# Optimization experiments

Hardware: AMD Instinct MI355X
Metric: run time of the kernel (lower is better)

Reference implementation:

```python
import jax, jax.numpy as jnp
import numpy as np

N_USERS = 6144
N_ITEMS = 12288
N_NODES = N_USERS + N_ITEMS
D = 64
AVG_DEG = 32
NNZ = N_NODES * AVG_DEG
N_LAYERS = 2
K = 30  # module keeps top (k+1) per row


def setup_inputs() -> dict:
    key = jax.random.key(0)
    k1, k2, k3, k4, k5 = jax.random.split(key, 5)
    user_emb = 0.1 * jax.random.normal(k1, (N_USERS, D), dtype=jnp.float32)
    item_emb = 0.1 * jax.random.normal(k2, (N_ITEMS, D), dtype=jnp.float32)
    edge_row = jax.random.randint(k3, (NNZ,), 0, N_NODES, dtype=jnp.int32)
    edge_col = jax.random.randint(k4, (NNZ,), 0, N_NODES, dtype=jnp.int32)
    # normalized-adjacency-like values (positive, ~1/deg scale)
    edge_val = jax.random.uniform(k5, (NNZ,), dtype=jnp.float32) / AVG_DEG
    return {
        "user_emb": user_emb,
        "item_emb": item_emb,
        "edge_row": edge_row,
        "edge_col": edge_col,
        "edge_val": edge_val,
    }


def _spmm(edge_row, edge_col, edge_val, x):
    # y[r] = sum_{(r,c) in E} val * x[c]   -- torch.sparse.mm equivalent (COO)
    return jax.ops.segment_sum(edge_val[:, None] * x[edge_col], edge_row,
                               num_segments=N_NODES)


def reference(user_emb, item_emb, edge_row, edge_col, edge_val):
    # LightGCN propagation
    all_emb = jnp.concatenate([user_emb, item_emb], axis=0)  # [N, D]
    embs = [all_emb]
    for _ in range(N_LAYERS):
        all_emb = _spmm(edge_row, edge_col, edge_val, all_emb)
        embs.append(all_emb)
    light_out = jnp.mean(jnp.stack(embs, axis=1), axis=1)  # [N, D]

    items = light_out[N_USERS:]  # [N_ITEMS, D]
    # F.normalize(dim=1, p=2) with eps clamp
    norm = jnp.linalg.norm(items, axis=1, keepdims=True)
    items = items / jnp.maximum(norm, 1e-12)

    # dense pairwise similarity
    sim = items @ items.T  # [N_ITEMS, N_ITEMS]

    # top_k: keep top (k+1) values per row, zero elsewhere
    vals, idx = jax.lax.top_k(sim, K + 1)  # [N_ITEMS, K+1]
    rows = jnp.arange(sim.shape[0])[:, None]
    sparse_sim = jnp.zeros_like(sim).at[rows, idx].set(vals)

    # apply_non_linearity('relu', i) -> relu
    return jax.nn.relu(sparse_sim)
```

## Files before the change

### kernel.cpp

```cpp
#include <hip/hip_runtime.h>
#include <hip/hip_bf16.h>

#define N_USERS 6144
#define N_ITEMS 12288
#define N_NODES 18432
#define D 64
#define NNZ 589824
#define K_TOP 31
#define NCAND_MIN 48
#define NCAND_MAX 240
#define CMAX 256

using frag_ab = __attribute__((ext_vector_type(8))) short;
using frag_cd = __attribute__((ext_vector_type(4))) float;

__device__ inline ushort f32_to_bf16_bits(float f) {
    unsigned b = __float_as_uint(f);
    unsigned r = (b + 0x7FFFu + ((b >> 16) & 1u)) >> 16;
    return (ushort)r;
}

__global__ void concat64_kernel(const float* __restrict__ u,
                                const float* __restrict__ it,
                                double* __restrict__ e0) {
    int i = blockIdx.x * 256 + threadIdx.x;
    const int NU = N_USERS * D;
    e0[i] = (i < NU) ? (double)u[i] : (double)it[i - NU];
}

__global__ void count_kernel(const int* __restrict__ er, int* __restrict__ cnt) {
    int e = blockIdx.x * 256 + threadIdx.x;
    atomicAdd(&cnt[er[e]], 1);
}

__global__ __launch_bounds__(256) void scan_kernel(const int* __restrict__ cnt,
                                                   int* __restrict__ row_start,
                                                   int* __restrict__ cursor) {
    __shared__ int part[256];
    int t = threadIdx.x;
    const int PER = N_NODES / 256;
    int s = 0;
    for (int i = 0; i < PER; ++i) s += cnt[t * PER + i];
    part[t] = s;
    __syncthreads();
    for (int off = 1; off < 256; off <<= 1) {
        int v = part[t];
        int w = (t >= off) ? part[t - off] : 0;
        __syncthreads();
        part[t] = v + w;
        __syncthreads();
    }
    int run = (t == 0) ? 0 : part[t - 1];
    for (int i = 0; i < PER; ++i) {
        int idx = t * PER + i;
        row_start[idx] = run;
        cursor[idx] = run;
        run += cnt[idx];
    }
    if (t == 255) row_start[N_NODES] = run;
}

__global__ void scatter_kernel(const int* __restrict__ er, const int* __restrict__ ec,
                               const float* __restrict__ ev,
                               int* __restrict__ cursor,
                               int* __restrict__ ecol_s, float* __restrict__ eval_s) {
    int e = blockIdx.x * 256 + threadIdx.x;
    int r = er[e];
    int pos = atomicAdd(&cursor[r], 1);
    ecol_s[pos] = ec[e];
    eval_s[pos] = ev[e];
}

__global__ __launch_bounds__(256) void spmm_csr_kernel(const int* __restrict__ row_start,
                                                       const int* __restrict__ ecol_s,
                                                       const float* __restrict__ eval_s,
                                                       const double* __restrict__ x,
                                                       double* __restrict__ y) {
    int t = threadIdx.x;
    int lane = t & 63, wave = t >> 6;
    int row = blockIdx.x * 4 + wave;
    if (row >= N_NODES) return;
    int beg = row_start[row], end = row_start[row + 1];
    double acc = 0.0;
    for (int j = beg; j < end; ++j) {
        int c = ecol_s[j];
        double v = (double)eval_s[j];
        acc += v * x[(size_t)c * D + lane];
    }
    y[(size_t)row * D + lane] = acc;
}

__global__ void mean_norm64_kernel(const double* __restrict__ e0,
                                   const double* __restrict__ e1,
                                   const double* __restrict__ e2,
                                   double* __restrict__ xn64,
                                   ushort* __restrict__ xh) {
    int t = threadIdx.x;
    int wave = t >> 6, lane = t & 63;
    int r = blockIdx.x * 4 + wave;
    size_t g = (size_t)(r + N_USERS) * D + lane;
    double s = (e0[g] + e1[g] + e2[g]) / 3.0;
    double ss = s * s;
    #pragma unroll
    for (int off = 32; off; off >>= 1) ss += __shfl_xor(ss, off);
    double norm = sqrt(ss);
    double denom = fmax(norm, 1e-12);
    double v = s / denom;
    xn64[(size_t)r * D + lane] = v;
    xh[(size_t)r * D + lane] = f32_to_bf16_bits((float)v);
}

#define LDS_STRIDE 72
__global__ __launch_bounds__(256) void simgemm_kernel(const ushort* __restrict__ Xh,
                                                      ushort* __restrict__ Cb) {
    __shared__ __align__(16) ushort Als[128 * LDS_STRIDE];
    __shared__ __align__(16) ushort Bls[128 * LDS_STRIDE];
    int t = threadIdx.x;
    int bi = blockIdx.y, bj = blockIdx.x;

    #pragma unroll
    for (int p = 0; p < 4; ++p) {
        int u4 = t + 256 * p;
        int row = u4 >> 3;
        int seg = u4 & 7;
        *(uint4*)&Als[row * LDS_STRIDE + seg * 8] =
            *(const uint4*)&Xh[(size_t)(bi * 128 + row) * D + seg * 8];
        *(uint4*)&Bls[row * LDS_STRIDE + seg * 8] =
            *(const uint4*)&Xh[(size_t)(bj * 128 + row) * D + seg * 8];
    }
    __syncthreads();

    int lane = t & 63, wave = t >> 6;
    int wrow = (wave >> 1) * 64, wcol = (wave & 1) * 64;
    int ml = lane & 15, quad = lane >> 4;

    frag_cd acc[4][4] = {};
    #pragma unroll
    for (int s = 0; s < 2; ++s) {
        frag_ab af[4], bf[4];
        int koff = s * 32 + quad * 8;
        #pragma unroll
        for (int rt = 0; rt < 4; ++rt)
            af[rt] = *(const frag_ab*)&Als[(wrow + rt * 16 + ml) * LDS_STRIDE + koff];
        #pragma unroll
        for (int ct = 0; ct < 4; ++ct)
            bf[ct] = *(const frag_ab*)&Bls[(wcol + ct * 16 + ml) * LDS_STRIDE + koff];
        #pragma unroll
        for (int rt = 0; rt < 4; ++rt)
            #pragma unroll
            for (int ct = 0; ct < 4; ++ct)
                acc[rt][ct] = __builtin_amdgcn_mfma_f32_16x16x32_bf16(
                    af[rt], bf[ct], acc[rt][ct], 0, 0, 0);
    }

    #pragma unroll
    for (int rt = 0; rt < 4; ++rt) {
        #pragma unroll
        for (int ct = 0; ct < 4; ++ct) {
            size_t gr = (size_t)(bi * 128 + wrow + rt * 16 + quad * 4);
            int    gc = bj * 128 + wcol + ct * 16 + ml;
            #pragma unroll
            for (int r = 0; r < 4; ++r)
                Cb[(gr + r) * N_ITEMS + gc] = f32_to_bf16_bits(acc[rt][ct][r]);
        }
    }
}

__global__ __launch_bounds__(256) void topk_kernel(const ushort* __restrict__ Cb,
                                                   float* __restrict__ Cout,
                                                   const double* __restrict__ xn64) {
    __shared__ int s_red[4];
    __shared__ unsigned s_cnt;
    __shared__ int    candi[CMAX];
    __shared__ double candv[CMAX];
    __shared__ double s_xr[D];
    int t = threadIdx.x;
    int r = blockIdx.x;
    const uint4* Crow4 = (const uint4*)(Cb + (size_t)r * N_ITEMS);

    unsigned short u[48];
    #pragma unroll
    for (int j = 0; j < 6; ++j) {
        uint4 f = Crow4[t + 256 * j];
        const unsigned* w = &f.x;
        #pragma unroll
        for (int q = 0; q < 4; ++q) {
            unsigned lo = w[q] & 0xFFFFu, hi = w[q] >> 16;
            u[j * 8 + 2 * q]     = (unsigned short)(lo ^ ((lo & 0x8000u) ? 0xFFFFu : 0x8000u));
            u[j * 8 + 2 * q + 1] = (unsigned short)(hi ^ ((hi & 0x8000u) ? 0xFFFFu : 0x8000u));
        }
    }
    if (t < D) s_xr[t] = xn64[(size_t)r * D + t];

    unsigned lo = 0u, hi = 0xFFFFu, T = 0u, bestT = 0u;
    int found = 0;
    for (int it = 0; it < 16; ++it) {
        if (found || lo > hi) { __syncthreads(); __syncthreads(); continue; }
        unsigned mid = lo + ((hi - lo) >> 1);
        int c = 0;
        #pragma unroll
        for (int k = 0; k < 48; ++k) c += (u[k] >= mid) ? 1 : 0;
        #pragma unroll
        for (int off = 32; off; off >>= 1) c += __shfl_down(c, off);
        if ((t & 63) == 0) s_red[t >> 6] = c;
        __syncthreads();
        int ctot = s_red[0] + s_red[1] + s_red[2] + s_red[3];
        __syncthreads();
        if (ctot >= NCAND_MIN) {
            bestT = mid;
            if (ctot <= NCAND_MAX) { T = mid; found = 1; }
            else lo = mid + 1;
        } else {
            if (mid == 0u) { lo = 1u; hi = 0u; }
            else hi = mid - 1;
        }
    }
    if (!found) T = bestT;

    if (t == 0) s_cnt = 0;
    __syncthreads();
    #pragma unroll
    for (int k = 0; k < 48; ++k) {
        if (u[k] >= (unsigned short)T) {
            unsigned pos = atomicAdd(&s_cnt, 1u);
            if (pos < CMAX) candi[pos] = 8 * (t + 256 * (k >> 3)) + (k & 7);
        }
    }
    __syncthreads();
    int c = (int)s_cnt; if (c > CMAX) c = CMAX;

    if (t < c) {
        const double* xc = xn64 + (size_t)candi[t] * D;
        double acc = 0.0;
        #pragma unroll 8
        for (int k = 0; k < D; ++k) acc += s_xr[k] * xc[k];
        candv[t] = acc;
    }
    __syncthreads();

    int   sel_idx = -1;
    float sel_val = 0.f;
    if (t < c) {
        double v = candv[t];
        int    id = candi[t];
        int rank = 0;
        for (int j = 0; j < c; ++j) {
            double vj = candv[j];
            rank += (vj > v || (vj == v && candi[j] < id)) ? 1 : 0;
        }
        if (rank < K_TOP) {
            sel_idx = id;
            sel_val = (v > 0.0) ? (float)v : 0.f;
        }
    }

    float4* Orow4 = (float4*)(Cout + (size_t)r * N_ITEMS);
    float4 z = make_float4(0.f, 0.f, 0.f, 0.f);
    #pragma unroll
    for (int j = 0; j < 12; ++j) Orow4[t + 256 * j] = z;
    __syncthreads();
    if (sel_idx >= 0) Cout[(size_t)r * N_ITEMS + sel_idx] = sel_val;
}

extern "C" void kernel_launch(void* const* d_in, const int* in_sizes, int n_in,
                              void* d_out, int out_size, void* d_ws, size_t ws_size,
                              hipStream_t stream) {
    const float* user_emb = (const float*)d_in[0];
    const float* item_emb = (const float*)d_in[1];
    const int*   edge_row = (const int*)d_in[2];
    const int*   edge_col = (const int*)d_in[3];
    const float* edge_val = (const float*)d_in[4];
    float* C = (float*)d_out;

    double* e0d  = (double*)d_ws;
    double* e1d  = e0d + (size_t)N_NODES * D;
    double* e2d  = e1d + (size_t)N_NODES * D;
    double* xn64 = e2d + (size_t)N_NODES * D;
    ushort* xh   = (ushort*)(xn64 + (size_t)N_ITEMS * D);
    ushort* Cb   = xh + (size_t)N_ITEMS * D;
    float*  eval_s = (float*)(Cb + (size_t)N_ITEMS * N_ITEMS);
    int*    ecol_s = (int*)(eval_s + NNZ);
    int*    cnt       = ecol_s + NNZ;
    int*    row_start = cnt + N_NODES;
    int*    cursor    = row_start + N_NODES + 1;

    hipMemsetAsync(cnt, 0, N_NODES * sizeof(int), stream);

    concat64_kernel<<<N_NODES * D / 256, 256, 0, stream>>>(user_emb, item_emb, e0d);

    count_kernel<<<NNZ / 256, 256, 0, stream>>>(edge_row, cnt);
    scan_kernel<<<1, 256, 0, stream>>>(cnt, row_start, cursor);
    scatter_kernel<<<NNZ / 256, 256, 0, stream>>>(edge_row, edge_col, edge_val,
                                                  cursor, ecol_s, eval_s);

    spmm_csr_kernel<<<(N_NODES + 3) / 4, 256, 0, stream>>>(row_start, ecol_s, eval_s, e0d, e1d);
    spmm_csr_kernel<<<(N_NODES + 3) / 4, 256, 0, stream>>>(row_start, ecol_s, eval_s, e1d, e2d);

    mean_norm64_kernel<<<N_ITEMS / 4, 256, 0, stream>>>(e0d, e1d, e2d, xn64, xh);

    dim3 ggrid(N_ITEMS / 128, N_ITEMS / 128);
    simgemm_kernel<<<ggrid, 256, 0, stream>>>(xh, Cb);

    topk_kernel<<<N_ITEMS, 256, 0, stream>>>(Cb, C, xn64);
}
```

Measured before the change: 1.004 ms.

## Pack edges, unroll SpMM, stage GEMM output via LDS, use nontemporal stores, early-exit search

Edge column and value are packed into one int2 array. The SpMM loop is unrolled by four with independent accumulators to raise memory-level parallelism. The similarity GEMM now writes its bf16 tile through LDS so that global stores are coalesced and nontemporal. The top-k kernel reads with nontemporal loads, zero-fills the output with nontemporal stores, and leaves the threshold binary search early, which is safe because the loop condition is uniform across the block. Splitting the sum into four accumulators changes the order of the double-precision additions slightly.

```diff
diff --git a/kernel.cpp b/kernel.cpp
--- a/kernel.cpp
+++ b/kernel.cpp
@@ -13,11 +13,13 @@
 
 using frag_ab = __attribute__((ext_vector_type(8))) short;
 using frag_cd = __attribute__((ext_vector_type(4))) float;
-
-__device__ inline ushort f32_to_bf16_bits(float f) {
+using uint4_e = __attribute__((ext_vector_type(4))) unsigned;
+using uint2_e = __attribute__((ext_vector_type(2))) unsigned;
+using float4_e = __attribute__((ext_vector_type(4))) float;
+
+__device__ inline unsigned f32_to_bf16_bits(float f) {
     unsigned b = __float_as_uint(f);
-    unsigned r = (b + 0x7FFFu + ((b >> 16) & 1u)) >> 16;
-    return (ushort)r;
+    return (b + 0x7FFFu + ((b >> 16) & 1u)) >> 16;
 }
 
 __global__ void concat64_kernel(const float* __restrict__ u,
@@ -62,18 +64,15 @@
 
 __global__ void scatter_kernel(const int* __restrict__ er, const int* __restrict__ ec,
                                const float* __restrict__ ev,
-                               int* __restrict__ cursor,
-                               int* __restrict__ ecol_s, float* __restrict__ eval_s) {
+                               int* __restrict__ cursor, int2* __restrict__ ep) {
     int e = blockIdx.x * 256 + threadIdx.x;
     int r = er[e];
     int pos = atomicAdd(&cursor[r], 1);
-    ecol_s[pos] = ec[e];
-    eval_s[pos] = ev[e];
+    ep[pos] = make_int2(ec[e], __float_as_int(ev[e]));
 }
 
 __global__ __launch_bounds__(256) void spmm_csr_kernel(const int* __restrict__ row_start,
-                                                       const int* __restrict__ ecol_s,
-                                                       const float* __restrict__ eval_s,
+                                                       const int2* __restrict__ ep,
                                                        const double* __restrict__ x,
                                                        double* __restrict__ y) {
     int t = threadIdx.x;
@@ -81,13 +80,21 @@
     int row = blockIdx.x * 4 + wave;
     if (row >= N_NODES) return;
     int beg = row_start[row], end = row_start[row + 1];
-    double acc = 0.0;
-    for (int j = beg; j < end; ++j) {
-        int c = ecol_s[j];
-        double v = (double)eval_s[j];
-        acc += v * x[(size_t)c * D + lane];
-    }
-    y[(size_t)row * D + lane] = acc;
+    double a0 = 0.0, a1 = 0.0, a2 = 0.0, a3 = 0.0;
+    int j = beg;
+    int n4 = beg + ((end - beg) & ~3);
+    for (; j < n4; j += 4) {
+        int2 p0 = ep[j], p1 = ep[j + 1], p2 = ep[j + 2], p3 = ep[j + 3];
+        a0 += (double)__int_as_float(p0.y) * x[(size_t)p0.x * D + lane];
+        a1 += (double)__int_as_float(p1.y) * x[(size_t)p1.x * D + lane];
+        a2 += (double)__int_as_float(p2.y) * x[(size_t)p2.x * D + lane];
+        a3 += (double)__int_as_float(p3.y) * x[(size_t)p3.x * D + lane];
+    }
+    for (; j < end; ++j) {
+        int2 p = ep[j];
+        a0 += (double)__int_as_float(p.y) * x[(size_t)p.x * D + lane];
+    }
+    y[(size_t)row * D + lane] = (a0 + a1) + (a2 + a3);
 }
 
 __global__ void mean_norm64_kernel(const double* __restrict__ e0,
@@ -107,14 +114,16 @@
     double denom = fmax(norm, 1e-12);
     double v = s / denom;
     xn64[(size_t)r * D + lane] = v;
-    xh[(size_t)r * D + lane] = f32_to_bf16_bits((float)v);
+    xh[(size_t)r * D + lane] = (ushort)f32_to_bf16_bits((float)v);
 }
 
 #define LDS_STRIDE 72
+#define OST_STRIDE 132
 __global__ __launch_bounds__(256) void simgemm_kernel(const ushort* __restrict__ Xh,
                                                       ushort* __restrict__ Cb) {
-    __shared__ __align__(16) ushort Als[128 * LDS_STRIDE];
-    __shared__ __align__(16) ushort Bls[128 * LDS_STRIDE];
+    __shared__ __align__(16) ushort S[2 * 128 * LDS_STRIDE];
+    ushort* Als = S;
+    ushort* Bls = S + 128 * LDS_STRIDE;
     int t = threadIdx.x;
     int bi = blockIdx.y, bj = blockIdx.x;
 
@@ -123,10 +132,10 @@
         int u4 = t + 256 * p;
         int row = u4 >> 3;
         int seg = u4 & 7;
-        *(uint4*)&Als[row * LDS_STRIDE + seg * 8] =
-            *(const uint4*)&Xh[(size_t)(bi * 128 + row) * D + seg * 8];
-        *(uint4*)&Bls[row * LDS_STRIDE + seg * 8] =
-            *(const uint4*)&Xh[(size_t)(bj * 128 + row) * D + seg * 8];
+        *(uint4_e*)&Als[row * LDS_STRIDE + seg * 8] =
+            *(const uint4_e*)&Xh[(size_t)(bi * 128 + row) * D + seg * 8];
+        *(uint4_e*)&Bls[row * LDS_STRIDE + seg * 8] =
+            *(const uint4_e*)&Xh[(size_t)(bj * 128 + row) * D + seg * 8];
     }
     __syncthreads();
 
@@ -152,17 +161,29 @@
                 acc[rt][ct] = __builtin_amdgcn_mfma_f32_16x16x32_bf16(
                     af[rt], bf[ct], acc[rt][ct], 0, 0, 0);
     }
-
+    __syncthreads();
+
+    ushort* Ost = S;
     #pragma unroll
     for (int rt = 0; rt < 4; ++rt) {
         #pragma unroll
         for (int ct = 0; ct < 4; ++ct) {
-            size_t gr = (size_t)(bi * 128 + wrow + rt * 16 + quad * 4);
-            int    gc = bj * 128 + wcol + ct * 16 + ml;
+            int row = wrow + rt * 16 + quad * 4;
+            int col = wcol + ct * 16 + ml;
             #pragma unroll
             for (int r = 0; r < 4; ++r)
-                Cb[(gr + r) * N_ITEMS + gc] = f32_to_bf16_bits(acc[rt][ct][r]);
-        }
+                Ost[(row + r) * OST_STRIDE + col] = (ushort)f32_to_bf16_bits(acc[rt][ct][r]);
+        }
+    }
+    __syncthreads();
+
+    const size_t base = (size_t)(bi * 128) * N_ITEMS + bj * 128;
+    #pragma unroll
+    for (int p = 0; p < 16; ++p) {
+        int i = t + 256 * p;
+        int row = i >> 5, cp = i & 31;
+        uint2_e v = *(const uint2_e*)&Ost[row * OST_STRIDE + cp * 4];
+        __builtin_nontemporal_store(v, (uint2_e*)(Cb + base + (size_t)row * N_ITEMS + cp * 4));
     }
 }
 
@@ -176,16 +197,16 @@
     __shared__ double s_xr[D];
     int t = threadIdx.x;
     int r = blockIdx.x;
-    const uint4* Crow4 = (const uint4*)(Cb + (size_t)r * N_ITEMS);
+    const uint4_e* Crow4 = (const uint4_e*)(Cb + (size_t)r * N_ITEMS);
 
     unsigned short u[48];
     #pragma unroll
     for (int j = 0; j < 6; ++j) {
-        uint4 f = Crow4[t + 256 * j];
-        const unsigned* w = &f.x;
+        uint4_e f = __builtin_nontemporal_load(&Crow4[t + 256 * j]);
         #pragma unroll
         for (int q = 0; q < 4; ++q) {
-            unsigned lo = w[q] & 0xFFFFu, hi = w[q] >> 16;
+            unsigned w = f[q];
+            unsigned lo = w & 0xFFFFu, hi = w >> 16;
             u[j * 8 + 2 * q]     = (unsigned short)(lo ^ ((lo & 0x8000u) ? 0xFFFFu : 0x8000u));
             u[j * 8 + 2 * q + 1] = (unsigned short)(hi ^ ((hi & 0x8000u) ? 0xFFFFu : 0x8000u));
         }
@@ -195,7 +216,6 @@
     unsigned lo = 0u, hi = 0xFFFFu, T = 0u, bestT = 0u;
     int found = 0;
     for (int it = 0; it < 16; ++it) {
-        if (found || lo > hi) { __syncthreads(); __syncthreads(); continue; }
         unsigned mid = lo + ((hi - lo) >> 1);
         int c = 0;
         #pragma unroll
@@ -211,9 +231,10 @@
             if (ctot <= NCAND_MAX) { T = mid; found = 1; }
             else lo = mid + 1;
         } else {
-            if (mid == 0u) { lo = 1u; hi = 0u; }
+            if (mid == 0u) { found = 1; T = bestT; }
             else hi = mid - 1;
         }
+        if (found || lo > hi) break;
     }
     if (!found) T = bestT;
 
@@ -254,10 +275,11 @@
         }
     }
 
-    float4* Orow4 = (float4*)(Cout + (size_t)r * N_ITEMS);
-    float4 z = make_float4(0.f, 0.f, 0.f, 0.f);
-    #pragma unroll
-    for (int j = 0; j < 12; ++j) Orow4[t + 256 * j] = z;
+    float4_e* Orow4 = (float4_e*)(Cout + (size_t)r * N_ITEMS);
+    float4_e z = {0.f, 0.f, 0.f, 0.f};
+    #pragma unroll
+    for (int j = 0; j < 12; ++j)
+        __builtin_nontemporal_store(z, &Orow4[t + 256 * j]);
     __syncthreads();
     if (sel_idx >= 0) Cout[(size_t)r * N_ITEMS + sel_idx] = sel_val;
 }
@@ -276,25 +298,23 @@
     double* e1d  = e0d + (size_t)N_NODES * D;
     double* e2d  = e1d + (size_t)N_NODES * D;
     double* xn64 = e2d + (size_t)N_NODES * D;
-    ushort* xh   = (ushort*)(xn64 + (size_t)N_ITEMS * D);
+    int2*   ep   = (int2*)(xn64 + (size_t)N_ITEMS * D);
+    ushort* xh   = (ushort*)(ep + NNZ);
     ushort* Cb   = xh + (size_t)N_ITEMS * D;
-    float*  eval_s = (float*)(Cb + (size_t)N_ITEMS * N_ITEMS);
-    int*    ecol_s = (int*)(eval_s + NNZ);
-    int*    cnt       = ecol_s + NNZ;
-    int*    row_start = cnt + N_NODES;
-    int*    cursor    = row_start + N_NODES + 1;
-
-    hipMemsetAsync(cnt, 0, N_NODES * sizeof(int), stream);
+    int*  cnt       = (int*)(Cb + (size_t)N_ITEMS * N_ITEMS);
+    int*  row_start = cnt + N_NODES;
+    int*  cursor    = row_start + N_NODES + 1;
+
+    (void)hipMemsetAsync(cnt, 0, N_NODES * sizeof(int), stream);
 
     concat64_kernel<<<N_NODES * D / 256, 256, 0, stream>>>(user_emb, item_emb, e0d);
 
     count_kernel<<<NNZ / 256, 256, 0, stream>>>(edge_row, cnt);
     scan_kernel<<<1, 256, 0, stream>>>(cnt, row_start, cursor);
-    scatter_kernel<<<NNZ / 256, 256, 0, stream>>>(edge_row, edge_col, edge_val,
-                                                  cursor, ecol_s, eval_s);
-
-    spmm_csr_kernel<<<(N_NODES + 3) / 4, 256, 0, stream>>>(row_start, ecol_s, eval_s, e0d, e1d);
-    spmm_csr_kernel<<<(N_NODES + 3) / 4, 256, 0, stream>>>(row_start, ecol_s, eval_s, e1d, e2d);
+    scatter_kernel<<<NNZ / 256, 256, 0, stream>>>(edge_row, edge_col, edge_val, cursor, ep);
+
+    spmm_csr_kernel<<<(N_NODES + 3) / 4, 256, 0, stream>>>(row_start, ep, e0d, e1d);
+    spmm_csr_kernel<<<(N_NODES + 3) / 4, 256, 0, stream>>>(row_start, ep, e1d, e2d);
 
     mean_norm64_kernel<<<N_ITEMS / 4, 256, 0, stream>>>(e0d, e1d, e2d, xn64, xh);
 
```

Measured after the change: 960.5 us. 1.05x faster.
